# Performance work log

Measured on AMD Instinct MI355X. Metric: run time of the kernel, lower is better.

## Reference

```python
import jax, jax.numpy as jnp
import numpy as np
import math

B, L = 2048, 60
D, H, NL = 80, 8, 3
HD = D // H            # head_dim = 10
NLOC, NUSR = 1187, 46
DFF = 2 * D
IN_DIM = D + 24 + 32 + 2   # loc(80)+user(24)+weekday(16)+hour(16)+2 continuous


def _ln(x, g, b):
    m = jnp.mean(x, -1, keepdims=True)
    v = jnp.mean((x - m) ** 2, -1, keepdims=True)
    return (x - m) * jax.lax.rsqrt(v + 1e-5) * g + b


def setup_inputs():
    key = jax.random.key(0)
    k = lambda i: jax.random.fold_in(key, i)
    g = lambda i, shp, s: jax.random.normal(k(i), shp, dtype=jnp.float32) * s
    inp = {
        "loc_seq": jax.random.randint(k(0), (B, L), 0, NLOC),
        "user_seq": jax.random.randint(k(1), (B, L), 0, NUSR),
        "weekday_seq": jax.random.randint(k(2), (B, L), 0, 8),
        "start_min_seq": jax.random.randint(k(3), (B, L), 0, 1440),
        "dur_seq": jax.random.randint(k(4), (B, L), 0, 600),
        "diff_seq": jax.random.randint(k(5), (B, L), 0, 100),
        "seq_len": jax.random.randint(k(6), (B,), 1, L + 1),
    }
    # embedding tables (padding_idx=0 rows zeroed where the module uses it)
    inp["loc_table"] = g(10, (NLOC, D), 0.02).at[0].set(0.0)
    inp["user_table"] = g(11, (NUSR, 24), 0.02).at[0].set(0.0)
    inp["wk_table"] = g(12, (8, 16), 0.02).at[0].set(0.0)
    inp["hr_table"] = g(13, (25, 16), 0.02)
    inp["in_w"] = g(14, (IN_DIM, D), 0.09)
    inp["in_b"] = jnp.zeros((D,), jnp.float32)
    inp["in_g"] = jnp.ones((D,), jnp.float32)
    inp["in_be"] = jnp.zeros((D,), jnp.float32)
    inp["pos_emb"] = g(15, (1, L, D), 0.02)
    # per-layer stacked params (NL=3 layers)
    inp["qkv_w"] = g(16, (NL, D, 3 * D), 0.09)
    inp["proj_w"] = g(17, (NL, D, D), 0.11)
    inp["proj_b"] = jnp.zeros((NL, D), jnp.float32)
    inp["rel_emb"] = g(18, (NL, 2 * L - 1, HD), 1.0)
    inp["n1_g"] = jnp.ones((NL, D), jnp.float32)
    inp["n1_b"] = jnp.zeros((NL, D), jnp.float32)
    inp["ffn_w1"] = g(19, (NL, D, DFF), 0.09)
    inp["ffn_b1"] = jnp.zeros((NL, DFF), jnp.float32)
    inp["ffn_w2"] = g(20, (NL, DFF, D), 0.09)
    inp["ffn_b2"] = jnp.zeros((NL, D), jnp.float32)
    inp["n2_g"] = jnp.ones((NL, D), jnp.float32)
    inp["n2_b"] = jnp.zeros((NL, D), jnp.float32)
    inp["fn_g"] = jnp.ones((D,), jnp.float32)
    inp["fn_b"] = jnp.zeros((D,), jnp.float32)
    inp["pr_w1"] = g(21, (D, D), 0.11)
    inp["pr_b1"] = jnp.zeros((D,), jnp.float32)
    inp["pr_w2"] = g(22, (D, NLOC), 0.04)
    inp["pr_b2"] = jnp.zeros((NLOC,), jnp.float32)
    inp["protos"] = g(23, (NLOC, D), 0.04)
    inp["temp"] = jnp.asarray(2.0, jnp.float32)
    return inp


def reference(loc_seq, user_seq, weekday_seq, start_min_seq, dur_seq, diff_seq, seq_len,
              loc_table, user_table, wk_table, hr_table, in_w, in_b, in_g, in_be, pos_emb,
              qkv_w, proj_w, proj_b, rel_emb, n1_g, n1_b, ffn_w1, ffn_b1, ffn_w2, ffn_b2,
              n2_g, n2_b, fn_g, fn_b, pr_w1, pr_b1, pr_w2, pr_b2, protos, temp):
    Bx, Lx = loc_seq.shape
    loc_e = loc_table[loc_seq]                                            # [B,L,80]
    user_e = jnp.broadcast_to(user_table[user_seq[:, 0]][:, None, :], (Bx, Lx, 24))
    hour = jnp.clip(start_min_seq // 60, 0, 23)
    cont = jnp.stack([diff_seq.astype(jnp.float32) / 10.0,
                      dur_seq.astype(jnp.float32) / 300.0], -1)           # [B,L,2]
    x = jnp.concatenate([loc_e, user_e, wk_table[weekday_seq], hr_table[hour], cont], -1)
    x = _ln(x @ in_w + in_b, in_g, in_be) + pos_emb[:, :Lx, :]
    key_mask = loc_seq == 0                                               # mask keys [B,L]
    pos_idx = jnp.arange(Lx)[None, :] - jnp.arange(Lx)[:, None] + (Lx - 1)  # [L,L]
    scale = 1.0 / math.sqrt(HD)
    for l in range(NL):
        qkv = (x @ qkv_w[l]).reshape(Bx, Lx, 3, H, HD)
        q = qkv[:, :, 0].transpose(0, 2, 1, 3)                            # [B,H,L,hd]
        kk = qkv[:, :, 1].transpose(0, 2, 1, 3)
        v = qkv[:, :, 2].transpose(0, 2, 1, 3)
        rel = rel_emb[l][pos_idx]                                         # [L,L,hd]
        attn = (jnp.einsum('bhid,bhjd->bhij', q, kk)
                + jnp.einsum('bhid,ijd->bhij', q, rel)) * scale
        attn = jnp.where(key_mask[:, None, None, :], -jnp.inf, attn)
        a = jax.nn.softmax(attn, -1)
        o = jnp.einsum('bhij,bhjd->bhid', a, v).transpose(0, 2, 1, 3).reshape(Bx, Lx, D)
        x = _ln(x + o @ proj_w[l] + proj_b[l], n1_g[l], n1_b[l])
        f = jax.nn.gelu(x @ ffn_w1[l] + ffn_b1[l], approximate=False) @ ffn_w2[l] + ffn_b2[l]
        x = _ln(x + f, n2_g[l], n2_b[l])
    x = _ln(x, fn_g, fn_b)
    final = x[jnp.arange(Bx), jnp.clip(seq_len - 1, 0, Lx - 1)]           # [B,80]
    logits_param = jax.nn.gelu(final @ pr_w1 + pr_b1, approximate=False) @ pr_w2 + pr_b2
    fnorm = final / jnp.maximum(jnp.linalg.norm(final, axis=-1, keepdims=True), 1e-12)
    pnorm = protos / jnp.maximum(jnp.linalg.norm(protos, axis=-1, keepdims=True), 1e-12)
    logits = 0.5 * logits_param + 0.5 * (fnorm @ pnorm.T) * 15.0
    return logits / jnp.clip(temp, 0.5, 3.0)
```

## Files before the change

kernel.cpp:

```cpp
#include <hip/hip_runtime.h>
#include <hip/hip_bf16.h>
#include <math.h>

#define BB   2048
#define LL   60
#define DD   80
#define HH   8
#define HDD  10
#define NLNUM 3
#define NLOC 1187
#define DFF  160
#define IN_DIM 138
#define RELN 119
#define SCS  68
#define XP   21
#define HP   41
#define VP   35

__device__ __forceinline__ float gelu_f(float a) {
  float x = fabsf(a) * 0.70710678118654752f;
  float t = 1.0f / (1.0f + 0.3275911f * x);
  float y = t * (0.254829592f + t * (-0.284496736f + t * (1.421413741f +
            t * (-1.453152027f + t * 1.061405429f))));
  float e = 1.0f - y * __expf(-x * x);
  float erf_s = copysignf(e, a);
  return 0.5f * a * (1.0f + erf_s);
}

__global__ __launch_bounds__(256) void k_embed(
    const int* __restrict__ loc_seq, const int* __restrict__ user_seq,
    const int* __restrict__ wk_seq, const int* __restrict__ sm_seq,
    const int* __restrict__ dur_seq, const int* __restrict__ diff_seq,
    const float* __restrict__ loc_table, const float* __restrict__ user_table,
    const float* __restrict__ wk_table, const float* __restrict__ hr_table,
    const float* __restrict__ in_w, const float* __restrict__ in_b,
    const float* __restrict__ in_g, const float* __restrict__ in_be,
    const float* __restrict__ pos_emb, float* __restrict__ x) {
  int tok0 = blockIdx.x * 48, tid = threadIdx.x;
  __shared__ __align__(16) float vin[48 * VP * 4];
  __shared__ __align__(16) float ws[140 * 80];
  __shared__ float mstd[96];

  float4* vin4 = (float4*)vin;
  float4* ws4  = (float4*)ws;

  for (int i = tid; i < 140 * 20; i += 256) {
    int r = i / 20, c = i % 20;
    float4 v = make_float4(0.0f, 0.0f, 0.0f, 0.0f);
    if (r < IN_DIM) v = *(const float4*)(in_w + r * 80 + c * 4);
    ws4[i] = v;
  }

  for (int i = tid; i < 48 * 35; i += 256) {
    int t = i / 35, s = i % 35;
    int tok = tok0 + t;
    float4 v;
    if (s < 20) {
      int loc = loc_seq[tok];
      v = *(const float4*)(loc_table + (size_t)loc * 80 + s * 4);
    } else if (s < 26) {
      int usr = user_seq[(tok / LL) * LL];
      v = *(const float4*)(user_table + usr * 24 + (s - 20) * 4);
    } else if (s < 30) {
      int wk = wk_seq[tok];
      v = *(const float4*)(wk_table + wk * 16 + (s - 26) * 4);
    } else if (s < 34) {
      int hr = sm_seq[tok] / 60; hr = min(max(hr, 0), 23);
      v = *(const float4*)(hr_table + hr * 16 + (s - 30) * 4);
    } else {
      v.x = (float)diff_seq[tok] / 10.0f;
      v.y = (float)dur_seq[tok] / 300.0f;
      v.z = 0.0f; v.w = 0.0f;
    }
    vin4[t * VP + s] = v;
  }
  __syncthreads();

  int tg = tid / 20, cg = tid % 20, t0 = tg * 4;
  float acc[4][4] = {};
  if (tid < 240) {
    #pragma unroll 7
    for (int iq = 0; iq < 35; iq++) {
      float4 xv[4], wv[4];
      #pragma unroll
      for (int dt = 0; dt < 4; dt++) xv[dt] = vin4[(t0 + dt) * VP + iq];
      #pragma unroll
      for (int di = 0; di < 4; di++) wv[di] = ws4[(iq * 4 + di) * 20 + cg];
      #pragma unroll
      for (int dt = 0; dt < 4; dt++) {
        const float* xp = (const float*)&xv[dt];
        #pragma unroll
        for (int di = 0; di < 4; di++) {
          const float* wp = (const float*)&wv[di];
          #pragma unroll
          for (int dc = 0; dc < 4; dc++) acc[dt][dc] += xp[di] * wp[dc];
        }
      }
    }
  }
  __syncthreads();
  if (tid < 240) {
    float4 bb = *(const float4*)(in_b + cg * 4);
    const float* bp = (const float*)&bb;
    #pragma unroll
    for (int dt = 0; dt < 4; dt++) {
      float4 y;
      y.x = acc[dt][0] + bp[0];
      y.y = acc[dt][1] + bp[1];
      y.z = acc[dt][2] + bp[2];
      y.w = acc[dt][3] + bp[3];
      vin4[(t0 + dt) * VP + cg] = y;
    }
  }
  __syncthreads();
  if (tid < 48) {
    float s = 0.0f, s2 = 0.0f;
    #pragma unroll
    for (int iq = 0; iq < 20; iq++) {
      float4 v = vin4[tid * VP + iq];
      s  += v.x + v.y + v.z + v.w;
      s2 += v.x * v.x + v.y * v.y + v.z * v.z + v.w * v.w;
    }
    float mean = s / 80.0f;
    float var  = fmaxf(s2 / 80.0f - mean * mean, 0.0f);
    mstd[tid] = mean; mstd[48 + tid] = rsqrtf(var + 1e-5f);
  }
  __syncthreads();
  for (int e = tid; e < 960; e += 256) {
    int t = e / 20, c4 = e % 20;
    float4 v = vin4[t * VP + c4];
    float4 gg = *(const float4*)(in_g + c4 * 4);
    float4 bb = *(const float4*)(in_be + c4 * 4);
    float4 pe = *(const float4*)(pos_emb + ((tok0 + t) % LL) * 80 + c4 * 4);
    float m = mstd[t], r = mstd[48 + t];
    float4 out;
    out.x = (v.x - m) * r * gg.x + bb.x + pe.x;
    out.y = (v.y - m) * r * gg.y + bb.y + pe.y;
    out.z = (v.z - m) * r * gg.z + bb.z + pe.z;
    out.w = (v.w - m) * r * gg.w + bb.w + pe.w;
    ((float4*)(x + (size_t)tok0 * 80))[e] = out;
  }
}

__global__ __launch_bounds__(256) void k_qkv(
    const float* __restrict__ x, const float* __restrict__ qkv_w,
    float* __restrict__ qkvo) {
  int b = blockIdx.x, tid = threadIdx.x;
  __shared__ __align__(16) float xs[LL * XP * 4];
  __shared__ __align__(16) float ws[DD * DD];

  const float4* xb4 = (const float4*)(x + (size_t)b * LL * DD);
  float4* xs4 = (float4*)xs;
  for (int i = tid; i < LL * 20; i += 256) xs4[(i / 20) * XP + (i % 20)] = xb4[i];
  float4* ws4 = (float4*)ws;

  for (int c0 = 0; c0 < 240; c0 += 80) {
    __syncthreads();
    for (int i = tid; i < 80 * 20; i += 256)
      ws4[i] = *(const float4*)(qkv_w + (i / 20) * 240 + c0 + (i % 20) * 4);
    __syncthreads();
    for (int slot = tid; slot < 300; slot += 256) {
      int tg = slot / 20, cg = slot % 20;
      int t0 = tg * 4;
      float acc[4][4] = {};
      #pragma unroll
      for (int iq = 0; iq < 20; iq++) {
        float4 xv[4], wv[4];
        #pragma unroll
        for (int dt = 0; dt < 4; dt++) xv[dt] = xs4[(t0 + dt) * XP + iq];
        #pragma unroll
        for (int di = 0; di < 4; di++) wv[di] = ws4[(iq * 4 + di) * 20 + cg];
        #pragma unroll
        for (int dt = 0; dt < 4; dt++) {
          const float* xp = (const float*)&xv[dt];
          #pragma unroll
          for (int di = 0; di < 4; di++) {
            const float* wp = (const float*)&wv[di];
            #pragma unroll
            for (int dc = 0; dc < 4; dc++) acc[dt][dc] += xp[di] * wp[dc];
          }
        }
      }
      float* qb = qkvo + (size_t)b * 14400 + (size_t)(c0 + cg * 4) * 60 + t0;
      #pragma unroll
      for (int dc = 0; dc < 4; dc++)
        *(float4*)(qb + dc * 60) = make_float4(acc[0][dc], acc[1][dc], acc[2][dc], acc[3][dc]);
    }
  }
}

__global__ __launch_bounds__(256) void k_attn(
    const float* __restrict__ qkvo, const int* __restrict__ loc_seq,
    const float* __restrict__ rel_emb,
    float* __restrict__ o) {
  int bh = blockIdx.x;
  int b = bh >> 3, h = bh & 7;
  int tid = threadIdx.x;

  __shared__ __align__(16) float qs[HDD * 60];
  __shared__ __align__(16) float ks[HDD * 60];
  __shared__ __align__(16) float vs[HDD * 60];
  __shared__ __align__(16) float relT[HDD * 120];
  __shared__ __align__(16) float sc[60 * SCS];
  __shared__ __align__(16) float rsum[64];
  __shared__ float msk[60];

  const float4* src = (const float4*)(qkvo + (size_t)b * 14400);
  float4* q4 = (float4*)qs; float4* k4 = (float4*)ks; float4* v4 = (float4*)vs;
  for (int i = tid; i < 150; i += 256) {
    q4[i] = src[h * 150 + i];
    k4[i] = src[1200 + h * 150 + i];
    v4[i] = src[2400 + h * 150 + i];
  }
  for (int i = tid; i < RELN * HDD; i += 256) {
    int d = i / RELN, p = i % RELN;
    relT[d * 120 + p] = rel_emb[p * 10 + d];
  }
  if (tid < 60) msk[tid] = (loc_seq[b * LL + tid] == 0) ? 1.0f : 0.0f;
  __syncthreads();

  if (tid < 225) {
    int ig = tid / 15, jg = tid % 15;
    int i0 = ig * 4, j0 = jg * 4;
    int w0 = j0 - i0 + 56;
    float acc[4][4] = {};
    #pragma unroll
    for (int d = 0; d < 10; d++) {
      float4 qv = *(const float4*)(qs + d * 60 + i0);
      float4 kv = *(const float4*)(ks + d * 60 + j0);
      float4 rA = *(const float4*)(relT + d * 120 + w0);
      float4 rB = *(const float4*)(relT + d * 120 + w0 + 4);
      float rr[8] = {rA.x, rA.y, rA.z, rA.w, rB.x, rB.y, rB.z, rB.w};
      const float* qp = (const float*)&qv;
      const float* kp = (const float*)&kv;
      #pragma unroll
      for (int di = 0; di < 4; di++)
        #pragma unroll
        for (int dj = 0; dj < 4; dj++)
          acc[di][dj] += qp[di] * (kp[dj] + rr[dj - di + 3]);
    }
    const float scale = 0.31622776601683794f;
    #pragma unroll
    for (int di = 0; di < 4; di++) {
      #pragma unroll
      for (int dj = 0; dj < 4; dj++) {
        float v = acc[di][dj] * scale;
        if (msk[j0 + dj] != 0.0f) v = -1e30f;
        acc[di][dj] = v;
      }
      *(float4*)(sc + (i0 + di) * SCS + j0) =
          make_float4(acc[di][0], acc[di][1], acc[di][2], acc[di][3]);
    }
  }
  __syncthreads();

  if (tid < 60) {
    float* row = sc + tid * SCS;
    int c = (tid >> 3) & 7;
    float m0 = -3.0e38f, m1 = -3.0e38f, m2 = -3.0e38f, m3 = -3.0e38f;
    #pragma unroll
    for (int s = 0; s < 15; s++) {
      int k = c + s; if (k >= 15) k -= 15;
      float4 v = *(const float4*)(row + 4 * k);
      m0 = fmaxf(m0, v.x); m1 = fmaxf(m1, v.y);
      m2 = fmaxf(m2, v.z); m3 = fmaxf(m3, v.w);
    }
    float m = fmaxf(fmaxf(m0, m1), fmaxf(m2, m3));
    float s0 = 0.0f, s1 = 0.0f, s2 = 0.0f, s3 = 0.0f;
    #pragma unroll
    for (int s = 0; s < 15; s++) {
      int k = c + s; if (k >= 15) k -= 15;
      float4 v = *(float4*)(row + 4 * k);
      v.x = __expf(v.x - m); v.y = __expf(v.y - m);
      v.z = __expf(v.z - m); v.w = __expf(v.w - m);
      *(float4*)(row + 4 * k) = v;
      s0 += v.x; s1 += v.y; s2 += v.z; s3 += v.w;
    }
    rsum[tid] = 1.0f / (s0 + s1 + s2 + s3);
  }
  __syncthreads();

  if (tid < 150) {
    int ig = tid / 10, d = tid % 10;
    float acc[4] = {0, 0, 0, 0};
    #pragma unroll 5
    for (int jq = 0; jq < 15; jq++) {
      float4 vv = *(const float4*)(vs + d * 60 + jq * 4);
      #pragma unroll
      for (int di = 0; di < 4; di++) {
        float4 av = *(const float4*)(sc + (ig + 15 * di) * SCS + jq * 4);
        acc[di] += av.x * vv.x + av.y * vv.y + av.z * vv.z + av.w * vv.w;
      }
    }
    #pragma unroll
    for (int di = 0; di < 4; di++) {
      float r = rsum[ig + 15 * di];
      o[((size_t)b * 60 + ig + 15 * di) * 80 + h * 10 + d] = acc[di] * r;
    }
  }
}

__global__ __launch_bounds__(256) void k_proj_ln(
    const float* __restrict__ o, const float* __restrict__ proj_w,
    const float* __restrict__ proj_b, const float* __restrict__ g,
    const float* __restrict__ be, float* __restrict__ x) {
  int tok0 = blockIdx.x * 48, tid = threadIdx.x;
  __shared__ __align__(16) float os[48 * XP * 4];
  __shared__ __align__(16) float ws[80 * 80];
  __shared__ float mstd[96];

  float4* os4 = (float4*)os;
  const float4* ob4 = (const float4*)(o + (size_t)tok0 * 80);
  for (int i = tid; i < 960; i += 256) os4[(i / 20) * XP + (i % 20)] = ob4[i];
  float4* ws4 = (float4*)ws;
  for (int i = tid; i < 1600; i += 256)
    ws4[i] = *(const float4*)(proj_w + (i / 20) * 80 + (i % 20) * 4);
  __syncthreads();

  int tg = tid / 20, cg = tid % 20, t0 = tg * 4;
  float acc[4][4] = {};
  if (tid < 240) {
    #pragma unroll
    for (int iq = 0; iq < 20; iq++) {
      float4 xv[4], wv[4];
      #pragma unroll
      for (int dt = 0; dt < 4; dt++) xv[dt] = os4[(t0 + dt) * XP + iq];
      #pragma unroll
      for (int di = 0; di < 4; di++) wv[di] = ws4[(iq * 4 + di) * 20 + cg];
      #pragma unroll
      for (int dt = 0; dt < 4; dt++) {
        const float* xp = (const float*)&xv[dt];
        #pragma unroll
        for (int di = 0; di < 4; di++) {
          const float* wp = (const float*)&wv[di];
          #pragma unroll
          for (int dc = 0; dc < 4; dc++) acc[dt][dc] += xp[di] * wp[dc];
        }
      }
    }
  }
  __syncthreads();
  if (tid < 240) {
    float4 pb = *(const float4*)(proj_b + cg * 4);
    const float* pbp = (const float*)&pb;
    #pragma unroll
    for (int dt = 0; dt < 4; dt++) {
      float4 xr = *(const float4*)(x + (size_t)(tok0 + t0 + dt) * 80 + cg * 4);
      const float* xrp = (const float*)&xr;
      float4 out;
      out.x = acc[dt][0] + pbp[0] + xrp[0];
      out.y = acc[dt][1] + pbp[1] + xrp[1];
      out.z = acc[dt][2] + pbp[2] + xrp[2];
      out.w = acc[dt][3] + pbp[3] + xrp[3];
      os4[(t0 + dt) * XP + cg] = out;
    }
  }
  __syncthreads();
  if (tid < 48) {
    float s = 0.0f, s2 = 0.0f;
    #pragma unroll
    for (int iq = 0; iq < 20; iq++) {
      float4 v = os4[tid * XP + iq];
      s  += v.x + v.y + v.z + v.w;
      s2 += v.x * v.x + v.y * v.y + v.z * v.z + v.w * v.w;
    }
    float mean = s / 80.0f;
    float var  = fmaxf(s2 / 80.0f - mean * mean, 0.0f);
    mstd[tid] = mean; mstd[48 + tid] = rsqrtf(var + 1e-5f);
  }
  __syncthreads();
  for (int e = tid; e < 960; e += 256) {
    int t = e / 20, c4 = e % 20;
    float4 v = os4[t * XP + c4];
    float4 gg = *(const float4*)(g + c4 * 4);
    float4 bb = *(const float4*)(be + c4 * 4);
    float m = mstd[t], r = mstd[48 + t];
    float4 out;
    out.x = (v.x - m) * r * gg.x + bb.x;
    out.y = (v.y - m) * r * gg.y + bb.y;
    out.z = (v.z - m) * r * gg.z + bb.z;
    out.w = (v.w - m) * r * gg.w + bb.w;
    ((float4*)(x + (size_t)tok0 * 80))[e] = out;
  }
}

__global__ __launch_bounds__(256) void k_ffn(
    const float* __restrict__ w1, const float* __restrict__ b1,
    const float* __restrict__ w2, const float* __restrict__ b2,
    const float* __restrict__ g, const float* __restrict__ be,
    float* __restrict__ x) {
  int tok0 = blockIdx.x * 48, tid = threadIdx.x;
  __shared__ __align__(16) float xs[48 * XP * 4];
  __shared__ __align__(16) float hs[48 * HP * 4];
  __shared__ __align__(16) float ws[80 * 80];
  __shared__ float mstd[96];

  float4* xs4 = (float4*)xs;
  float4* hs4 = (float4*)hs;
  float4* ws4 = (float4*)ws;
  const float4* xb4 = (const float4*)(x + (size_t)tok0 * 80);
  for (int i = tid; i < 960; i += 256) xs4[(i / 20) * XP + (i % 20)] = xb4[i];

  int tg = tid / 20, cg = tid % 20, t0 = tg * 4;

  for (int c0 = 0; c0 < 160; c0 += 80) {
    __syncthreads();
    for (int i = tid; i < 1600; i += 256)
      ws4[i] = *(const float4*)(w1 + (i / 20) * 160 + c0 + (i % 20) * 4);
    __syncthreads();
    if (tid < 240) {
      float acc[4][4] = {};
      #pragma unroll
      for (int iq = 0; iq < 20; iq++) {
        float4 xv[4], wv[4];
        #pragma unroll
        for (int dt = 0; dt < 4; dt++) xv[dt] = xs4[(t0 + dt) * XP + iq];
        #pragma unroll
        for (int di = 0; di < 4; di++) wv[di] = ws4[(iq * 4 + di) * 20 + cg];
        #pragma unroll
        for (int dt = 0; dt < 4; dt++) {
          const float* xp = (const float*)&xv[dt];
          #pragma unroll
          for (int di = 0; di < 4; di++) {
            const float* wp = (const float*)&wv[di];
            #pragma unroll
            for (int dc = 0; dc < 4; dc++) acc[dt][dc] += xp[di] * wp[dc];
          }
        }
      }
      float4 bb = *(const float4*)(b1 + c0 + cg * 4);
      const float* bp = (const float*)&bb;
      #pragma unroll
      for (int dt = 0; dt < 4; dt++) {
        float4 out;
        float* op = (float*)&out;
        #pragma unroll
        for (int dc = 0; dc < 4; dc++)
          op[dc] = gelu_f(acc[dt][dc] + bp[dc]);
        hs4[(t0 + dt) * HP + c0 / 4 + cg] = out;
      }
    }
  }

  float acc[4][4] = {};
  for (int k0 = 0; k0 < 160; k0 += 80) {
    __syncthreads();
    for (int i = tid; i < 1600; i += 256)
      ws4[i] = *(const float4*)(w2 + (size_t)(k0 + i / 20) * 80 + (i % 20) * 4);
    __syncthreads();
    if (tid < 240) {
      #pragma unroll
      for (int iq = 0; iq < 20; iq++) {
        float4 hv[4], wv[4];
        #pragma unroll
        for (int dt = 0; dt < 4; dt++) hv[dt] = hs4[(t0 + dt) * HP + k0 / 4 + iq];
        #pragma unroll
        for (int di = 0; di < 4; di++) wv[di] = ws4[(iq * 4 + di) * 20 + cg];
        #pragma unroll
        for (int dt = 0; dt < 4; dt++) {
          const float* hp = (const float*)&hv[dt];
          #pragma unroll
          for (int di = 0; di < 4; di++) {
            const float* wp = (const float*)&wv[di];
            #pragma unroll
            for (int dc = 0; dc < 4; dc++) acc[dt][dc] += hp[di] * wp[dc];
          }
        }
      }
    }
  }
  __syncthreads();
  if (tid < 240) {
    float4 bb = *(const float4*)(b2 + cg * 4);
    const float* bp = (const float*)&bb;
    #pragma unroll
    for (int dt = 0; dt < 4; dt++) {
      float4 xr = xs4[(t0 + dt) * XP + cg];
      const float* xrp = (const float*)&xr;
      float4 out;
      out.x = acc[dt][0] + bp[0] + xrp[0];
      out.y = acc[dt][1] + bp[1] + xrp[1];
      out.z = acc[dt][2] + bp[2] + xrp[2];
      out.w = acc[dt][3] + bp[3] + xrp[3];
      hs4[(t0 + dt) * HP + cg] = out;
    }
  }
  __syncthreads();
  if (tid < 48) {
    float s = 0.0f, s2 = 0.0f;
    #pragma unroll
    for (int iq = 0; iq < 20; iq++) {
      float4 v = hs4[tid * HP + iq];
      s  += v.x + v.y + v.z + v.w;
      s2 += v.x * v.x + v.y * v.y + v.z * v.z + v.w * v.w;
    }
    float mean = s / 80.0f;
    float var  = fmaxf(s2 / 80.0f - mean * mean, 0.0f);
    mstd[tid] = mean; mstd[48 + tid] = rsqrtf(var + 1e-5f);
  }
  __syncthreads();
  for (int e = tid; e < 960; e += 256) {
    int t = e / 20, c4 = e % 20;
    float4 v = hs4[t * HP + c4];
    float4 gg = *(const float4*)(g + c4 * 4);
    float4 bb = *(const float4*)(be + c4 * 4);
    float m = mstd[t], r = mstd[48 + t];
    float4 out;
    out.x = (v.x - m) * r * gg.x + bb.x;
    out.y = (v.y - m) * r * gg.y + bb.y;
    out.z = (v.z - m) * r * gg.z + bb.z;
    out.w = (v.w - m) * r * gg.w + bb.w;
    ((float4*)(x + (size_t)tok0 * 80))[e] = out;
  }
}

__global__ __launch_bounds__(128) void k_final(
    const float* __restrict__ x, const int* __restrict__ seq_len,
    const float* __restrict__ fn_g, const float* __restrict__ fn_b,
    const float* __restrict__ pr_w1, const float* __restrict__ pr_b1,
    float* __restrict__ fnorm, float* __restrict__ h1) {
  int b = blockIdx.x, tid = threadIdx.x;
  __shared__ float red[128], red2[128];
  __shared__ float fbuf[DD];
  int t = seq_len[b] - 1; t = min(max(t, 0), LL - 1);
  float v = 0.0f;
  if (tid < DD) v = x[((size_t)b * LL + t) * DD + tid];
  red[tid]  = (tid < DD) ? v : 0.0f;
  red2[tid] = (tid < DD) ? v * v : 0.0f;
  __syncthreads();
  for (int s = 64; s > 0; s >>= 1) {
    if (tid < s) { red[tid] += red[tid + s]; red2[tid] += red2[tid + s]; }
    __syncthreads();
  }
  float mean = red[0] / DD;
  float var  = fmaxf(red2[0] / DD - mean * mean, 0.0f);
  float rstd = rsqrtf(var + 1e-5f);
  float f = 0.0f;
  if (tid < DD) { f = (v - mean) * rstd * fn_g[tid] + fn_b[tid]; fbuf[tid] = f; }
  __syncthreads();
  red[tid] = (tid < DD) ? f * f : 0.0f;
  __syncthreads();
  for (int s = 64; s > 0; s >>= 1) {
    if (tid < s) red[tid] += red[tid + s];
    __syncthreads();
  }
  float rn = 1.0f / fmaxf(sqrtf(red[0]), 1e-12f);
  if (tid < DD) {
    fnorm[(size_t)b * DD + tid] = f * rn;
    float gacc = pr_b1[tid];
    for (int i = 0; i < DD; i++) gacc += fbuf[i] * pr_w1[i * DD + tid];
    h1[(size_t)b * DD + tid] = gelu_f(gacc);
  }
}

__global__ __launch_bounds__(128) void k_pnorm(
    const float* __restrict__ protos, float* __restrict__ pnormT) {
  int c = blockIdx.x, tid = threadIdx.x;
  __shared__ float red[128];
  float v = 0.0f;
  if (tid < DD) v = protos[(size_t)c * DD + tid];
  red[tid] = (tid < DD) ? v * v : 0.0f;
  __syncthreads();
  for (int s = 64; s > 0; s >>= 1) {
    if (tid < s) red[tid] += red[tid + s];
    __syncthreads();
  }
  float rn = 1.0f / fmaxf(sqrtf(red[0]), 1e-12f);
  if (tid < DD) pnormT[(size_t)tid * NLOC + c] = v * rn;
}

__global__ __launch_bounds__(256) void k_logits(
    const float* __restrict__ h1, const float* __restrict__ fnorm,
    const float* __restrict__ pr_w2, const float* __restrict__ pr_b2,
    const float* __restrict__ pnormT, const float* __restrict__ temp,
    float* __restrict__ out) {
  int b = blockIdx.x / 5, cb = blockIdx.x % 5;
  int tid = threadIdx.x;
  int c = cb * 256 + tid;
  __shared__ float h1s[DD], fns[DD];
  if (tid < DD) { h1s[tid] = h1[(size_t)b * DD + tid]; fns[tid] = fnorm[(size_t)b * DD + tid]; }
  __syncthreads();
  if (c < NLOC) {
    float a1 = pr_b2[c], a2 = 0.0f;
    for (int k = 0; k < DD; k++) {
      a1 += h1s[k] * pr_w2[(size_t)k * NLOC + c];
      a2 += fns[k] * pnormT[(size_t)k * NLOC + c];
    }
    float tt = fminf(fmaxf(temp[0], 0.5f), 3.0f);
    out[(size_t)b * NLOC + c] = (0.5f * a1 + 7.5f * a2) / tt;
  }
}

extern "C" void kernel_launch(void* const* d_in, const int* in_sizes, int n_in,
                              void* d_out, int out_size, void* d_ws, size_t ws_size,
                              hipStream_t stream) {
  const int* loc_seq   = (const int*)d_in[0];
  const int* user_seq  = (const int*)d_in[1];
  const int* wk_seq    = (const int*)d_in[2];
  const int* sm_seq    = (const int*)d_in[3];
  const int* dur_seq   = (const int*)d_in[4];
  const int* diff_seq  = (const int*)d_in[5];
  const int* seq_len   = (const int*)d_in[6];
  const float* loc_table = (const float*)d_in[7];
  const float* user_table= (const float*)d_in[8];
  const float* wk_table  = (const float*)d_in[9];
  const float* hr_table  = (const float*)d_in[10];
  const float* in_w   = (const float*)d_in[11];
  const float* in_b   = (const float*)d_in[12];
  const float* in_g   = (const float*)d_in[13];
  const float* in_be  = (const float*)d_in[14];
  const float* pos_emb= (const float*)d_in[15];
  const float* qkv_w  = (const float*)d_in[16];
  const float* proj_w = (const float*)d_in[17];
  const float* proj_b = (const float*)d_in[18];
  const float* rel_emb= (const float*)d_in[19];
  const float* n1_g   = (const float*)d_in[20];
  const float* n1_b   = (const float*)d_in[21];
  const float* ffn_w1 = (const float*)d_in[22];
  const float* ffn_b1 = (const float*)d_in[23];
  const float* ffn_w2 = (const float*)d_in[24];
  const float* ffn_b2 = (const float*)d_in[25];
  const float* n2_g   = (const float*)d_in[26];
  const float* n2_b   = (const float*)d_in[27];
  const float* fn_g   = (const float*)d_in[28];
  const float* fn_b   = (const float*)d_in[29];
  const float* pr_w1  = (const float*)d_in[30];
  const float* pr_b1  = (const float*)d_in[31];
  const float* pr_w2  = (const float*)d_in[32];
  const float* pr_b2  = (const float*)d_in[33];
  const float* protos = (const float*)d_in[34];
  const float* temp   = (const float*)d_in[35];
  float* out = (float*)d_out;

  float* x      = (float*)d_ws;
  float* o      = x + (size_t)BB * LL * DD;
  float* qkvo   = o + (size_t)BB * LL * DD;
  float* fnorm  = qkvo + (size_t)BB * 14400;
  float* h1     = fnorm + (size_t)BB * DD;
  float* pnormT = h1 + (size_t)BB * DD;

  k_embed<<<BB * LL / 48, 256, 0, stream>>>(loc_seq, user_seq, wk_seq, sm_seq,
                                            dur_seq, diff_seq, loc_table,
                                            user_table, wk_table, hr_table,
                                            in_w, in_b, in_g, in_be, pos_emb, x);

  for (int l = 0; l < NLNUM; l++) {
    k_qkv<<<BB, 256, 0, stream>>>(x, qkv_w + (size_t)l * 80 * 240, qkvo);
    k_attn<<<BB * HH, 256, 0, stream>>>(qkvo, loc_seq,
                                        rel_emb + (size_t)l * RELN * HDD, o);
    k_proj_ln<<<BB * LL / 48, 256, 0, stream>>>(o, proj_w + (size_t)l * DD * DD,
                                                proj_b + (size_t)l * DD,
                                                n1_g + (size_t)l * DD,
                                                n1_b + (size_t)l * DD, x);
    k_ffn<<<BB * LL / 48, 256, 0, stream>>>(ffn_w1 + (size_t)l * DD * DFF,
                                            ffn_b1 + (size_t)l * DFF,
                                            ffn_w2 + (size_t)l * DFF * DD,
                                            ffn_b2 + (size_t)l * DD,
                                            n2_g + (size_t)l * DD,
                                            n2_b + (size_t)l * DD, x);
  }

  k_pnorm<<<NLOC, 128, 0, stream>>>(protos, pnormT);
  k_final<<<BB, 128, 0, stream>>>(x, seq_len, fn_g, fn_b, pr_w1, pr_b1, fnorm, h1);
  k_logits<<<BB * 5, 256, 0, stream>>>(h1, fnorm, pr_w2, pr_b2, pnormT, temp, out);
}
```

Measured before the change: 1.686 ms.

## Fuse QKV projection into per-batch attention kernel looping over heads

```diff
diff --git a/kernel.cpp b/kernel.cpp
--- a/kernel.cpp
+++ b/kernel.cpp
@@ -27,6 +27,20 @@
   return 0.5f * a * (1.0f + erf_s);
 }
 
+__global__ __launch_bounds__(256) void k_wprep(
+    const float* __restrict__ qkv_w, float* __restrict__ wT) {
+  int idx = blockIdx.x * 256 + threadIdx.x;
+  if (idx >= 3 * 8 * 30 * 80) return;
+  int i = idx % 80;
+  int c = (idx / 80) % 30;
+  int h = (idx / (80 * 30)) % 8;
+  int l = idx / (80 * 30 * 8);
+  int col = (c < 10) ? (h * 10 + c)
+          : (c < 20) ? (80 + h * 10 + (c - 10))
+                     : (160 + h * 10 + (c - 20));
+  wT[idx] = qkv_w[(size_t)l * 80 * 240 + (size_t)i * 240 + col];
+}
+
 __global__ __launch_bounds__(256) void k_embed(
     const int* __restrict__ loc_seq, const int* __restrict__ user_seq,
     const int* __restrict__ wk_seq, const int* __restrict__ sm_seq,
@@ -50,7 +64,6 @@
     if (r < IN_DIM) v = *(const float4*)(in_w + r * 80 + c * 4);
     ws4[i] = v;
   }
-
   for (int i = tid; i < 48 * 35; i += 256) {
     int t = i / 35, s = i % 35;
     int tok = tok0 + t;
@@ -142,162 +155,162 @@
   }
 }
 
-__global__ __launch_bounds__(256) void k_qkv(
-    const float* __restrict__ x, const float* __restrict__ qkv_w,
-    float* __restrict__ qkvo) {
-  int b = blockIdx.x, tid = threadIdx.x;
-  __shared__ __align__(16) float xs[LL * XP * 4];
-  __shared__ __align__(16) float ws[DD * DD];
-
-  const float4* xb4 = (const float4*)(x + (size_t)b * LL * DD);
-  float4* xs4 = (float4*)xs;
-  for (int i = tid; i < LL * 20; i += 256) xs4[(i / 20) * XP + (i % 20)] = xb4[i];
-  float4* ws4 = (float4*)ws;
-
-  for (int c0 = 0; c0 < 240; c0 += 80) {
-    __syncthreads();
-    for (int i = tid; i < 80 * 20; i += 256)
-      ws4[i] = *(const float4*)(qkv_w + (i / 20) * 240 + c0 + (i % 20) * 4);
-    __syncthreads();
-    for (int slot = tid; slot < 300; slot += 256) {
-      int tg = slot / 20, cg = slot % 20;
-      int t0 = tg * 4;
-      float acc[4][4] = {};
-      #pragma unroll
-      for (int iq = 0; iq < 20; iq++) {
-        float4 xv[4], wv[4];
-        #pragma unroll
-        for (int dt = 0; dt < 4; dt++) xv[dt] = xs4[(t0 + dt) * XP + iq];
-        #pragma unroll
-        for (int di = 0; di < 4; di++) wv[di] = ws4[(iq * 4 + di) * 20 + cg];
-        #pragma unroll
-        for (int dt = 0; dt < 4; dt++) {
-          const float* xp = (const float*)&xv[dt];
-          #pragma unroll
-          for (int di = 0; di < 4; di++) {
-            const float* wp = (const float*)&wv[di];
-            #pragma unroll
-            for (int dc = 0; dc < 4; dc++) acc[dt][dc] += xp[di] * wp[dc];
-          }
-        }
-      }
-      float* qb = qkvo + (size_t)b * 14400 + (size_t)(c0 + cg * 4) * 60 + t0;
-      #pragma unroll
-      for (int dc = 0; dc < 4; dc++)
-        *(float4*)(qb + dc * 60) = make_float4(acc[0][dc], acc[1][dc], acc[2][dc], acc[3][dc]);
-    }
-  }
-}
-
-__global__ __launch_bounds__(256) void k_attn(
-    const float* __restrict__ qkvo, const int* __restrict__ loc_seq,
+__global__ __launch_bounds__(256) void k_battn(
+    const float* __restrict__ x, const int* __restrict__ loc_seq,
+    const float* __restrict__ wT,
     const float* __restrict__ rel_emb,
     float* __restrict__ o) {
-  int bh = blockIdx.x;
-  int b = bh >> 3, h = bh & 7;
-  int tid = threadIdx.x;
-
-  __shared__ __align__(16) float qs[HDD * 60];
-  __shared__ __align__(16) float ks[HDD * 60];
-  __shared__ __align__(16) float vs[HDD * 60];
+  int b = blockIdx.x, tid = threadIdx.x;
+
+  __shared__ __align__(16) float xs[LL * XP * 4];
+  __shared__ __align__(16) float wsl[30 * XP * 4];
+  __shared__ __align__(16) float qkvh[30 * 60];
   __shared__ __align__(16) float relT[HDD * 120];
-  __shared__ __align__(16) float sc[60 * SCS];
+  __shared__ __align__(16) float sc[LL * SCS];
+  __shared__ __align__(16) float os[LL * XP * 4];
   __shared__ __align__(16) float rsum[64];
   __shared__ float msk[60];
 
-  const float4* src = (const float4*)(qkvo + (size_t)b * 14400);
-  float4* q4 = (float4*)qs; float4* k4 = (float4*)ks; float4* v4 = (float4*)vs;
-  for (int i = tid; i < 150; i += 256) {
-    q4[i] = src[h * 150 + i];
-    k4[i] = src[1200 + h * 150 + i];
-    v4[i] = src[2400 + h * 150 + i];
-  }
+  float4* xs4  = (float4*)xs;
+  float4* wsl4 = (float4*)wsl;
+  float4* os4  = (float4*)os;
+
+  const float4* xb4 = (const float4*)(x + (size_t)b * 4800);
+  for (int i = tid; i < 1200; i += 256) xs4[(i / 20) * XP + (i % 20)] = xb4[i];
   for (int i = tid; i < RELN * HDD; i += 256) {
     int d = i / RELN, p = i % RELN;
     relT[d * 120 + p] = rel_emb[p * 10 + d];
   }
   if (tid < 60) msk[tid] = (loc_seq[b * LL + tid] == 0) ? 1.0f : 0.0f;
-  __syncthreads();
-
-  if (tid < 225) {
-    int ig = tid / 15, jg = tid % 15;
-    int i0 = ig * 4, j0 = jg * 4;
-    int w0 = j0 - i0 + 56;
-    float acc[4][4] = {};
-    #pragma unroll
-    for (int d = 0; d < 10; d++) {
-      float4 qv = *(const float4*)(qs + d * 60 + i0);
-      float4 kv = *(const float4*)(ks + d * 60 + j0);
-      float4 rA = *(const float4*)(relT + d * 120 + w0);
-      float4 rB = *(const float4*)(relT + d * 120 + w0 + 4);
-      float rr[8] = {rA.x, rA.y, rA.z, rA.w, rB.x, rB.y, rB.z, rB.w};
-      const float* qp = (const float*)&qv;
-      const float* kp = (const float*)&kv;
-      #pragma unroll
-      for (int di = 0; di < 4; di++)
-        #pragma unroll
-        for (int dj = 0; dj < 4; dj++)
-          acc[di][dj] += qp[di] * (kp[dj] + rr[dj - di + 3]);
-    }
-    const float scale = 0.31622776601683794f;
-    #pragma unroll
-    for (int di = 0; di < 4; di++) {
-      #pragma unroll
-      for (int dj = 0; dj < 4; dj++) {
-        float v = acc[di][dj] * scale;
-        if (msk[j0 + dj] != 0.0f) v = -1e30f;
-        acc[di][dj] = v;
-      }
-      *(float4*)(sc + (i0 + di) * SCS + j0) =
-          make_float4(acc[di][0], acc[di][1], acc[di][2], acc[di][3]);
-    }
-  }
-  __syncthreads();
-
-  if (tid < 60) {
-    float* row = sc + tid * SCS;
-    int c = (tid >> 3) & 7;
-    float m0 = -3.0e38f, m1 = -3.0e38f, m2 = -3.0e38f, m3 = -3.0e38f;
-    #pragma unroll
-    for (int s = 0; s < 15; s++) {
-      int k = c + s; if (k >= 15) k -= 15;
-      float4 v = *(const float4*)(row + 4 * k);
-      m0 = fmaxf(m0, v.x); m1 = fmaxf(m1, v.y);
-      m2 = fmaxf(m2, v.z); m3 = fmaxf(m3, v.w);
-    }
-    float m = fmaxf(fmaxf(m0, m1), fmaxf(m2, m3));
-    float s0 = 0.0f, s1 = 0.0f, s2 = 0.0f, s3 = 0.0f;
-    #pragma unroll
-    for (int s = 0; s < 15; s++) {
-      int k = c + s; if (k >= 15) k -= 15;
-      float4 v = *(float4*)(row + 4 * k);
-      v.x = __expf(v.x - m); v.y = __expf(v.y - m);
-      v.z = __expf(v.z - m); v.w = __expf(v.w - m);
-      *(float4*)(row + 4 * k) = v;
-      s0 += v.x; s1 += v.y; s2 += v.z; s3 += v.w;
-    }
-    rsum[tid] = 1.0f / (s0 + s1 + s2 + s3);
-  }
-  __syncthreads();
-
-  if (tid < 150) {
-    int ig = tid / 10, d = tid % 10;
-    float acc[4] = {0, 0, 0, 0};
-    #pragma unroll 5
-    for (int jq = 0; jq < 15; jq++) {
-      float4 vv = *(const float4*)(vs + d * 60 + jq * 4);
+
+  for (int h = 0; h < HH; h++) {
+    __syncthreads();
+    const float4* w4 = (const float4*)(wT + (size_t)h * 2400);
+    for (int i = tid; i < 600; i += 256) wsl4[(i / 20) * XP + (i % 20)] = w4[i];
+    __syncthreads();
+
+    if (tid < 225) {
+      int ct = tid / 15, tt = tid % 15;
+      int c2 = ct * 2, t0 = tt * 4;
+      float acc[2][4] = {};
+      #pragma unroll 5
+      for (int iq = 0; iq < 20; iq++) {
+        float4 wv0 = wsl4[c2 * XP + iq];
+        float4 wv1 = wsl4[(c2 + 1) * XP + iq];
+        const float* w0 = (const float*)&wv0;
+        const float* w1 = (const float*)&wv1;
+        #pragma unroll
+        for (int dt = 0; dt < 4; dt++) {
+          float4 xv = xs4[(t0 + dt) * XP + iq];
+          const float* xp = (const float*)&xv;
+          #pragma unroll
+          for (int di = 0; di < 4; di++) {
+            acc[0][dt] += w0[di] * xp[di];
+            acc[1][dt] += w1[di] * xp[di];
+          }
+        }
+      }
+      *(float4*)(qkvh + c2 * 60 + t0) =
+          make_float4(acc[0][0], acc[0][1], acc[0][2], acc[0][3]);
+      *(float4*)(qkvh + (c2 + 1) * 60 + t0) =
+          make_float4(acc[1][0], acc[1][1], acc[1][2], acc[1][3]);
+    }
+    __syncthreads();
+
+    const float* qs = qkvh;
+    const float* ks = qkvh + 600;
+    if (tid < 225) {
+      int ig = tid / 15, jg = tid % 15;
+      int i0 = ig * 4, j0 = jg * 4;
+      int w0 = j0 - i0 + 56;
+      float acc[4][4] = {};
+      #pragma unroll
+      for (int d = 0; d < 10; d++) {
+        float4 qv = *(const float4*)(qs + d * 60 + i0);
+        float4 kv = *(const float4*)(ks + d * 60 + j0);
+        float4 rA = *(const float4*)(relT + d * 120 + w0);
+        float4 rB = *(const float4*)(relT + d * 120 + w0 + 4);
+        float rr[8] = {rA.x, rA.y, rA.z, rA.w, rB.x, rB.y, rB.z, rB.w};
+        const float* qp = (const float*)&qv;
+        const float* kp = (const float*)&kv;
+        #pragma unroll
+        for (int di = 0; di < 4; di++)
+          #pragma unroll
+          for (int dj = 0; dj < 4; dj++)
+            acc[di][dj] += qp[di] * (kp[dj] + rr[dj - di + 3]);
+      }
+      const float scale = 0.31622776601683794f;
       #pragma unroll
       for (int di = 0; di < 4; di++) {
-        float4 av = *(const float4*)(sc + (ig + 15 * di) * SCS + jq * 4);
-        acc[di] += av.x * vv.x + av.y * vv.y + av.z * vv.z + av.w * vv.w;
-      }
-    }
-    #pragma unroll
-    for (int di = 0; di < 4; di++) {
-      float r = rsum[ig + 15 * di];
-      o[((size_t)b * 60 + ig + 15 * di) * 80 + h * 10 + d] = acc[di] * r;
-    }
-  }
+        #pragma unroll
+        for (int dj = 0; dj < 4; dj++) {
+          float v = acc[di][dj] * scale;
+          if (msk[j0 + dj] != 0.0f) v = -1e30f;
+          acc[di][dj] = v;
+        }
+        *(float4*)(sc + (i0 + di) * SCS + j0) =
+            make_float4(acc[di][0], acc[di][1], acc[di][2], acc[di][3]);
+      }
+    }
+    __syncthreads();
+
+    if (tid < 240) {
+      int r = tid >> 2, q = tid & 3;
+      float* row = sc + r * SCS;
+      float4 vbuf[4];
+      float m = -3.0e38f;
+      #pragma unroll
+      for (int s = 0; s < 4; s++) {
+        int k = q + 4 * s;
+        if (k < 15) {
+          float4 v = *(const float4*)(row + 4 * k);
+          vbuf[s] = v;
+          m = fmaxf(m, fmaxf(fmaxf(v.x, v.y), fmaxf(v.z, v.w)));
+        }
+      }
+      m = fmaxf(m, __shfl_xor(m, 1));
+      m = fmaxf(m, __shfl_xor(m, 2));
+      float sum = 0.0f;
+      #pragma unroll
+      for (int s = 0; s < 4; s++) {
+        int k = q + 4 * s;
+        if (k < 15) {
+          float4 v = vbuf[s];
+          v.x = __expf(v.x - m); v.y = __expf(v.y - m);
+          v.z = __expf(v.z - m); v.w = __expf(v.w - m);
+          *(float4*)(row + 4 * k) = v;
+          sum += v.x + v.y + v.z + v.w;
+        }
+      }
+      sum += __shfl_xor(sum, 1);
+      sum += __shfl_xor(sum, 2);
+      if (q == 0) rsum[r] = 1.0f / sum;
+    }
+    __syncthreads();
+
+    if (tid < 150) {
+      int ig = tid / 10, d = tid % 10;
+      const float* vsr = qkvh + 1200 + d * 60;
+      float acc[4] = {0, 0, 0, 0};
+      #pragma unroll 5
+      for (int jq = 0; jq < 15; jq++) {
+        float4 vv = *(const float4*)(vsr + jq * 4);
+        #pragma unroll
+        for (int di = 0; di < 4; di++) {
+          float4 av = *(const float4*)(sc + (ig + 15 * di) * SCS + jq * 4);
+          acc[di] += av.x * vv.x + av.y * vv.y + av.z * vv.z + av.w * vv.w;
+        }
+      }
+      #pragma unroll
+      for (int di = 0; di < 4; di++) {
+        int t = ig + 15 * di;
+        os[t * (XP * 4) + h * 10 + d] = acc[di] * rsum[t];
+      }
+    }
+  }
+  __syncthreads();
+  float4* ob4 = (float4*)(o + (size_t)b * 4800);
+  for (int i = tid; i < 1200; i += 256) ob4[i] = os4[(i / 20) * XP + (i % 20)];
 }
 
 __global__ __launch_bounds__(256) void k_proj_ln(
@@ -634,10 +647,12 @@
 
   float* x      = (float*)d_ws;
   float* o      = x + (size_t)BB * LL * DD;
-  float* qkvo   = o + (size_t)BB * LL * DD;
-  float* fnorm  = qkvo + (size_t)BB * 14400;
+  float* wT     = o + (size_t)BB * LL * DD;
+  float* fnorm  = wT + 57600;
   float* h1     = fnorm + (size_t)BB * DD;
   float* pnormT = h1 + (size_t)BB * DD;
+
+  k_wprep<<<225, 256, 0, stream>>>(qkv_w, wT);
 
   k_embed<<<BB * LL / 48, 256, 0, stream>>>(loc_seq, user_seq, wk_seq, sm_seq,
                                             dur_seq, diff_seq, loc_table,
@@ -645,9 +660,8 @@
                                             in_w, in_b, in_g, in_be, pos_emb, x);
 
   for (int l = 0; l < NLNUM; l++) {
-    k_qkv<<<BB, 256, 0, stream>>>(x, qkv_w + (size_t)l * 80 * 240, qkvo);
-    k_attn<<<BB * HH, 256, 0, stream>>>(qkvo, loc_seq,
-                                        rel_emb + (size_t)l * RELN * HDD, o);
+    k_battn<<<BB, 256, 0, stream>>>(x, loc_seq, wT + (size_t)l * 8 * 30 * 80,
+                                    rel_emb + (size_t)l * RELN * HDD, o);
     k_proj_ln<<<BB * LL / 48, 256, 0, stream>>>(o, proj_w + (size_t)l * DD * DD,
                                                 proj_b + (size_t)l * DD,
                                                 n1_g + (size_t)l * DD,
```

After: 1.728 ms. +2.5%, slower.
